# Performance work log

Measured on AMD Instinct MI355X. Metric: run time of the kernel, lower is better.

## Reference

```python
import jax, jax.numpy as jnp
import numpy as np

N_NODES = 100000
N_EDGES = 800000
HIDDEN = 128


def setup_inputs() -> dict:
    key = jax.random.key(0)
    ks = jax.random.split(key, 9)
    h_n = jax.random.normal(ks[0], (N_NODES, HIDDEN), dtype=jnp.float32)
    edge_src = jax.random.randint(ks[1], (N_EDGES,), 0, N_NODES, dtype=jnp.int32)
    edge_dst = jax.random.randint(ks[2], (N_EDGES,), 0, N_NODES, dtype=jnp.int32)
    s = 0.05
    W_w = jax.random.normal(ks[3], (HIDDEN, HIDDEN), dtype=jnp.float32) * s
    W_b = jax.random.normal(ks[4], (HIDDEN,), dtype=jnp.float32) * s
    Ws_w = jax.random.normal(ks[5], (HIDDEN, HIDDEN), dtype=jnp.float32) * s
    Ws_b = jax.random.normal(ks[6], (HIDDEN,), dtype=jnp.float32) * s
    Wt_w = jax.random.normal(ks[7], (HIDDEN, HIDDEN), dtype=jnp.float32) * s
    Wt_b = jax.random.normal(ks[8], (HIDDEN,), dtype=jnp.float32) * s
    return {"h_n": h_n, "edge_src": edge_src, "edge_dst": edge_dst,
            "W_w": W_w, "W_b": W_b, "Ws_w": Ws_w, "Ws_b": Ws_b,
            "Wt_w": Wt_w, "Wt_b": Wt_b}


def reference(h_n, edge_src, edge_dst, W_w, W_b, Ws_w, Ws_b, Wt_w, Wt_b):
    # Dense linears (nn.Linear: x @ W.T + b)
    Wh = h_n @ W_w.T + W_b        # [N,H] used for A @ W(h)
    Wsh = h_n @ Ws_w.T + Ws_b     # [N,H] self term
    Wth = h_n @ Wt_w.T + Wt_b     # [N,H] used for A.T @ W_trans(h)
    # A[src,dst] = 1:  (A @ X)[i]   = sum over edges (i,j) of X[j]
    #              (A.T @ X)[j] = sum over edges (i,j) of X[i]
    agg_fwd = jax.ops.segment_sum(Wh[edge_dst], edge_src, num_segments=N_NODES)
    agg_bwd = jax.ops.segment_sum(Wth[edge_src], edge_dst, num_segments=N_NODES)
    return jax.nn.relu(agg_fwd + Wsh + agg_bwd)
```

## Files before the change

kernel.cpp:

```cpp
#include <hip/hip_runtime.h>
#include <hip/hip_bf16.h>

#define NN 100000
#define NE 800000
#define HIDDEN 128
#define NED (2 * NE)
#define BKN 64
#define NBF 1563
#define NBUCK (2 * NBF)
#define PS 13
#define CHUNK 4096
#define PBLK ((NED + CHUNK - 1) / CHUNK)
#define NTILES 3125

typedef __attribute__((ext_vector_type(8))) short bf16x8;
typedef __attribute__((ext_vector_type(4))) short bf16x4;
typedef __attribute__((ext_vector_type(4))) float f32x4;

__device__ __forceinline__ short f2bf(float f) {
  union { float f; unsigned u; } x; x.f = f;
  unsigned r = x.u + 0x7fffu + ((x.u >> 16) & 1u);
  return (short)(r >> 16);
}
__device__ __forceinline__ float bf2f(short s) {
  union { unsigned u; float f; } x;
  x.u = ((unsigned)(unsigned short)s) << 16;
  return x.f;
}

__global__ __launch_bounds__(256) void convert_weights(
    const float* __restrict__ m0, const float* __restrict__ m1,
    const float* __restrict__ m2, short* __restrict__ out) {
  int i = blockIdx.x * 256 + threadIdx.x;
  int m = i >> 14, j = i & 16383;
  const float* s = (m == 0) ? m0 : (m == 1) ? m1 : m2;
  out[i] = f2bf(s[j]);
}

__global__ __launch_bounds__(256) void convert_h(
    const float* __restrict__ h, short* __restrict__ h_bf) {
  int i = blockIdx.x * 256 + threadIdx.x;
  f32x4 v = *(const f32x4*)(h + (size_t)i * 4);
  bf16x4 o;
#pragma unroll
  for (int j = 0; j < 4; j++) o[j] = f2bf(v[j]);
  *(bf16x4*)(h_bf + (size_t)i * 4) = o;
}

__global__ __launch_bounds__(256) void part_count(
    const int* __restrict__ esrc, const int* __restrict__ edst,
    int* __restrict__ ghist) {
  __shared__ int lh[NBUCK];
  int tid = threadIdx.x;
  for (int i = tid; i < NBUCK; i += 256) lh[i] = 0;
  __syncthreads();
  int base = blockIdx.x * CHUNK;
  int nit = min(CHUNK, NED - base);
  for (int k = tid; k < nit; k += 256) {
    int ed = base + k;
    int b;
    if (ed < NE) b = esrc[ed] >> 6;
    else b = NBF + (edst[ed - NE] >> 6);
    atomicAdd(&lh[b], 1);
  }
  __syncthreads();
  for (int i = tid; i < NBUCK; i += 256) {
    int c = lh[i];
    if (c) atomicAdd(ghist + i, c);
  }
}

__global__ __launch_bounds__(1024) void bucket_scan(
    const int* __restrict__ ghist, int* __restrict__ bstart,
    int* __restrict__ gcur) {
  __shared__ int wsum[16];
  __shared__ int woff[16];
  int tid = threadIdx.x;
  int lane = tid & 63, wv = tid >> 6;
  int base = tid * 4;
  int v0 = (base + 0 < NBUCK) ? ghist[base + 0] : 0;
  int v1 = (base + 1 < NBUCK) ? ghist[base + 1] : 0;
  int v2 = (base + 2 < NBUCK) ? ghist[base + 2] : 0;
  int v3 = (base + 3 < NBUCK) ? ghist[base + 3] : 0;
  int s = v0 + v1 + v2 + v3;
  int inc = s;
#pragma unroll
  for (int d = 1; d < 64; d <<= 1) {
    int t = __shfl_up(inc, d, 64);
    if (lane >= d) inc += t;
  }
  if (lane == 63) wsum[wv] = inc;
  __syncthreads();
  if (wv == 0) {
    int x = (lane < 16) ? wsum[lane] : 0;
    int i2 = x;
#pragma unroll
    for (int d = 1; d < 16; d <<= 1) {
      int t = __shfl_up(i2, d, 64);
      if (lane >= d) i2 += t;
    }
    if (lane < 16) woff[lane] = i2 - x;
  }
  __syncthreads();
  int e = woff[wv] + inc - s;
  if (base + 0 < NBUCK) { bstart[base + 0] = e; gcur[base + 0] = e; }
  e += v0;
  if (base + 1 < NBUCK) { bstart[base + 1] = e; gcur[base + 1] = e; }
  e += v1;
  if (base + 2 < NBUCK) { bstart[base + 2] = e; gcur[base + 2] = e; }
  e += v2;
  if (base + 3 < NBUCK) { bstart[base + 3] = e; gcur[base + 3] = e; }
  e += v3;
  if (tid == 1023) bstart[NBUCK] = e;
}

__global__ __launch_bounds__(256) void part_scatter(
    const int* __restrict__ esrc, const int* __restrict__ edst,
    int* __restrict__ gcur, unsigned* __restrict__ ELP) {
  __shared__ int lcur[NBUCK];
  __shared__ int loff[NBUCK];
  __shared__ int gbase[NBUCK];
  __shared__ int psum[256];
  __shared__ unsigned buf[CHUNK];
  __shared__ unsigned short bidA[CHUNK];
  int tid = threadIdx.x;
  for (int i = tid; i < NBUCK; i += 256) lcur[i] = 0;
  __syncthreads();
  int base = blockIdx.x * CHUNK;
  int nit = min(CHUNK, NED - base);
  for (int k = tid; k < nit; k += 256) {
    int ed = base + k;
    int b;
    if (ed < NE) b = esrc[ed] >> 6;
    else b = NBF + (edst[ed - NE] >> 6);
    atomicAdd(&lcur[b], 1);
  }
  __syncthreads();
  int s = 0;
  int lo0 = tid * PS, hi0 = min(NBUCK, tid * PS + PS);
  for (int j = lo0; j < hi0; j++) s += lcur[j];
  psum[tid] = s;
  __syncthreads();
  for (int off = 1; off < 256; off <<= 1) {
    int x = psum[tid];
    int add = (tid >= off) ? psum[tid - off] : 0;
    __syncthreads();
    psum[tid] = x + add;
    __syncthreads();
  }
  int run = psum[tid] - s;
  for (int j = lo0; j < hi0; j++) { loff[j] = run; run += lcur[j]; }
  __syncthreads();
  for (int b = tid; b < NBUCK; b += 256) {
    int c = lcur[b];
    if (c) gbase[b] = atomicAdd(gcur + b, c);
    lcur[b] = loff[b];
  }
  __syncthreads();
  for (int k = tid; k < nit; k += 256) {
    int ed = base + k;
    int b, tl, nbr;
    if (ed < NE) { int tg = esrc[ed]; nbr = edst[ed]; b = tg >> 6; tl = tg & 63; }
    else { int e = ed - NE; int tg = edst[e]; nbr = esrc[e]; b = NBF + (tg >> 6); tl = tg & 63; }
    int slot = atomicAdd(&lcur[b], 1);
    buf[slot] = ((unsigned)tl << 17) | (unsigned)nbr;
    bidA[slot] = (unsigned short)b;
  }
  __syncthreads();
  for (int i = tid; i < nit; i += 256) {
    int b = bidA[i];
    ELP[gbase[b] + (i - loff[b])] = buf[i];
  }
}

#define ACC8(V) { a0f+=bf2f((V)[0]); a1f+=bf2f((V)[1]); a2f+=bf2f((V)[2]); a3f+=bf2f((V)[3]); \
                  a4f+=bf2f((V)[4]); a5f+=bf2f((V)[5]); a6f+=bf2f((V)[6]); a7f+=bf2f((V)[7]); }
#define MACC8(M,V) { a0f=fmaf(M,bf2f((V)[0]),a0f); a1f=fmaf(M,bf2f((V)[1]),a1f); \
                     a2f=fmaf(M,bf2f((V)[2]),a2f); a3f=fmaf(M,bf2f((V)[3]),a3f); \
                     a4f=fmaf(M,bf2f((V)[4]),a4f); a5f=fmaf(M,bf2f((V)[5]),a5f); \
                     a6f=fmaf(M,bf2f((V)[6]),a6f); a7f=fmaf(M,bf2f((V)[7]),a7f); }
__global__ __launch_bounds__(256, 6) void bucket_gather(
    const short* __restrict__ h_bf, const unsigned* __restrict__ ELP,
    const int* __restrict__ bstart,
    short* __restrict__ aggF, short* __restrict__ aggB,
    int* __restrict__ degFB) {
  __shared__ int sorted[1024];
  __shared__ int cnt[BKN];
  __shared__ int pfx[BKN];
  __shared__ int cur[BKN];
  int tid = threadIdx.x;
  int blk = blockIdx.x;
  int s = bstart[blk], e = bstart[blk + 1], n = e - s;
  if (tid < BKN) cnt[tid] = 0;
  __syncthreads();
  for (int k = tid; k < n; k += 256) atomicAdd(&cnt[ELP[s + k] >> 17], 1);
  __syncthreads();
  int v = (tid < BKN) ? cnt[tid] : 0;
  if (tid < BKN) pfx[tid] = v;
  __syncthreads();
  for (int off = 1; off < BKN; off <<= 1) {
    int add = (tid < BKN && tid >= off) ? pfx[tid - off] : 0;
    __syncthreads();
    if (tid < BKN) pfx[tid] += add;
    __syncthreads();
  }
  if (tid < BKN) cur[tid] = pfx[tid] - cnt[tid];
  __syncthreads();
  for (int k = tid; k < n; k += 256) {
    unsigned pv = ELP[s + k];
    int slot = atomicAdd(&cur[pv >> 17], 1);
    sorted[slot] = (int)(pv & 0x1FFFFu);
  }
  __syncthreads();
  int dir = blk >= NBF;
  int node0 = (dir ? blk - NBF : blk) * BKN;
  short* agg = dir ? aggB : aggF;
  int qw = tid >> 4, q = tid & 15;
  const short* hb = h_bf + (size_t)q * 8;
#pragma unroll
  for (int t = 0; t < 4; t++) {
    int nd = qw * 4 + t;
    int b0 = pfx[nd];
    int deg = cnt[nd];
    int a0 = b0 - deg;
    float a0f = 0.f, a1f = 0.f, a2f = 0.f, a3f = 0.f;
    float a4f = 0.f, a5f = 0.f, a6f = 0.f, a7f = 0.f;
    if (deg > 0) {
      int lastp = b0 - 1;
      int i0 = sorted[a0];
      int i1 = sorted[min(a0 + 1, lastp)];
      int i2 = sorted[min(a0 + 2, lastp)];
      int i3 = sorted[min(a0 + 3, lastp)];
      bf16x8 v0 = *(const bf16x8*)(hb + (size_t)i0 * HIDDEN);
      bf16x8 v1 = *(const bf16x8*)(hb + (size_t)i1 * HIDDEN);
      bf16x8 v2 = *(const bf16x8*)(hb + (size_t)i2 * HIDDEN);
      bf16x8 v3 = *(const bf16x8*)(hb + (size_t)i3 * HIDDEN);
      int j = a0;
      int ni0 = sorted[min(j + 4, lastp)];
      int ni1 = sorted[min(j + 5, lastp)];
      int ni2 = sorted[min(j + 6, lastp)];
      int ni3 = sorted[min(j + 7, lastp)];
      while (j + 4 <= b0) {
        ACC8(v0); v0 = *(const bf16x8*)(hb + (size_t)ni0 * HIDDEN);
        ACC8(v1); v1 = *(const bf16x8*)(hb + (size_t)ni1 * HIDDEN);
        ACC8(v2); v2 = *(const bf16x8*)(hb + (size_t)ni2 * HIDDEN);
        ACC8(v3); v3 = *(const bf16x8*)(hb + (size_t)ni3 * HIDDEN);
        j += 4;
        ni0 = sorted[min(j + 4, lastp)];
        ni1 = sorted[min(j + 5, lastp)];
        ni2 = sorted[min(j + 6, lastp)];
        ni3 = sorted[min(j + 7, lastp)];
      }
      int r = b0 - j;
      float m1 = (r > 0) ? 1.f : 0.f;
      float m2 = (r > 1) ? 1.f : 0.f;
      float m3 = (r > 2) ? 1.f : 0.f;
      MACC8(m1, v0); MACC8(m2, v1); MACC8(m3, v2);
    }
    int node = node0 + nd;
    if (node < NN) {
      bf16x8 o;
      o[0] = f2bf(a0f); o[1] = f2bf(a1f); o[2] = f2bf(a2f); o[3] = f2bf(a3f);
      o[4] = f2bf(a4f); o[5] = f2bf(a5f); o[6] = f2bf(a6f); o[7] = f2bf(a7f);
      *(bf16x8*)(agg + (size_t)node * HIDDEN + q * 8) = o;
    }
  }
  if (tid < BKN) {
    int node = node0 + tid;
    if (node < NN) degFB[dir * NN + node] = cnt[tid];
  }
}

__global__ __launch_bounds__(512, 4) void gemm_fused(
    const short* __restrict__ h_bf, const short* __restrict__ aggF,
    const short* __restrict__ aggB, const short* __restrict__ Wbf,
    const float* __restrict__ Wb, const float* __restrict__ Wsb,
    const float* __restrict__ Wtb, const int* __restrict__ degFB,
    float* __restrict__ out) {
  __shared__ short At[3 * 32 * 136];
  int tid = threadIdx.x;
  int lane = tid & 63;
  int m16 = lane & 15;
  int kq  = lane >> 4;
  int col0 = (tid >> 6) * 16;

  bf16x8 wf[3][4];
#pragma unroll
  for (int i = 0; i < 3; i++)
#pragma unroll
    for (int t = 0; t < 4; t++)
      wf[i][t] = *(const bf16x8*)(Wbf + i * 16384 + (col0 + m16) * 128 + t * 32 + kq * 8);

  f32x4 bW = *(const f32x4*)(Wb  + col0 + kq * 4);
  f32x4 bS = *(const f32x4*)(Wsb + col0 + kq * 4);
  f32x4 bT = *(const f32x4*)(Wtb + col0 + kq * 4);

  int srow = tid >> 4, skc = tid & 15;
  const short* mats[3] = { h_bf, aggF, aggB };
  const short* gbs[3];
  short* lps[3];
#pragma unroll
  for (int k = 0; k < 3; k++) {
    gbs[k] = mats[k] + srow * 128 + skc * 8;
    lps[k] = At + k * 4352 + srow * 136 + skc * 8;
  }

  int tile = blockIdx.x;
  bf16x8 ld[3];
#pragma unroll
  for (int k = 0; k < 3; k++)
    ld[k] = *(const bf16x8*)(gbs[k] + (size_t)tile * 4096);

  while (tile < NTILES) {
    int row0 = tile * 32;
    __syncthreads();
#pragma unroll
    for (int k = 0; k < 3; k++) *(bf16x8*)lps[k] = ld[k];
    __syncthreads();
    int ntile = tile + gridDim.x;
    if (ntile < NTILES) {
#pragma unroll
      for (int k = 0; k < 3; k++)
        ld[k] = *(const bf16x8*)(gbs[k] + (size_t)ntile * 4096);
    }
#pragma unroll
    for (int g = 0; g < 2; g++) {
      f32x4 acc = {0.f, 0.f, 0.f, 0.f};
      const short* lb = At + (g * 16 + m16) * 136 + kq * 8;
#pragma unroll
      for (int i = 0; i < 3; i++)
#pragma unroll
        for (int t = 0; t < 4; t++) {
          bf16x8 af = *(const bf16x8*)(lb + i * 4352 + t * 32);
          acc = __builtin_amdgcn_mfma_f32_16x16x32_bf16(wf[i][t], af, acc, 0, 0, 0);
        }
      int r = row0 + g * 16 + m16;
      float dF = (float)degFB[r];
      float dB = (float)degFB[NN + r];
      f32x4 v;
#pragma unroll
      for (int j = 0; j < 4; j++)
        v[j] = fmaxf(acc[j] + bS[j] + dF * bW[j] + dB * bT[j], 0.f);
      *(f32x4*)(out + (size_t)r * HIDDEN + col0 + kq * 4) = v;
    }
    tile = ntile;
  }
}

extern "C" void kernel_launch(void* const* d_in, const int* in_sizes, int n_in,
                              void* d_out, int out_size, void* d_ws, size_t ws_size,
                              hipStream_t stream) {
  const float* h    = (const float*)d_in[0];
  const int*   esrc = (const int*)d_in[1];
  const int*   edst = (const int*)d_in[2];
  const float* Ww   = (const float*)d_in[3];
  const float* Wb   = (const float*)d_in[4];
  const float* Wsw  = (const float*)d_in[5];
  const float* Wsb  = (const float*)d_in[6];
  const float* Wtw  = (const float*)d_in[7];
  const float* Wtb  = (const float*)d_in[8];
  float* out = (float*)d_out;

  char* ws = (char*)d_ws;
  int*      ghist  = (int*)(ws + 0);
  int*      bstart = (int*)(ws + 12544);
  int*      gcur   = (int*)(ws + 25088);
  unsigned* ELP    = (unsigned*)(ws + 37632);
  short*    Wbf    = (short*)(ws + 6437632);
  short*    h_bf   = (short*)(ws + 6535936);
  short*    aggF   = (short*)(ws + 32135936);
  short*    aggB   = (short*)(ws + 57735936);
  int*      degFB  = (int*)(ws + 83335936);

  hipMemsetAsync(ghist, 0, NBUCK * sizeof(int), stream);

  convert_weights<<<192, 256, 0, stream>>>(Wsw, Ww, Wtw, Wbf);
  convert_h<<<12500, 256, 0, stream>>>(h, h_bf);
  part_count<<<PBLK, 256, 0, stream>>>(esrc, edst, ghist);
  bucket_scan<<<1, 1024, 0, stream>>>(ghist, bstart, gcur);
  part_scatter<<<PBLK, 256, 0, stream>>>(esrc, edst, gcur, ELP);
  bucket_gather<<<NBUCK, 256, 0, stream>>>(h_bf, ELP, bstart, aggF, aggB, degFB);
  gemm_fused<<<1024, 512, 0, stream>>>(
      h_bf, aggF, aggB, Wbf, Wb, Wsb, Wtb, degFB, out);
}
```

Baseline: 258.7 us.

## Fuse bucket gather with GEMM epilogue, merging forward and backward buckets per node block

New measurement: 260.6 us. Within noise of the previous version (+0.8%).

```diff
diff --git a/kernel.cpp b/kernel.cpp
--- a/kernel.cpp
+++ b/kernel.cpp
@@ -7,11 +7,10 @@
 #define NED (2 * NE)
 #define BKN 64
 #define NBF 1563
-#define NBUCK (2 * NBF)
-#define PS 13
+#define NBUCK NBF
+#define PS 7
 #define CHUNK 4096
 #define PBLK ((NED + CHUNK - 1) / CHUNK)
-#define NTILES 3125
 
 typedef __attribute__((ext_vector_type(8))) short bf16x8;
 typedef __attribute__((ext_vector_type(4))) short bf16x4;
@@ -58,9 +57,7 @@
   int nit = min(CHUNK, NED - base);
   for (int k = tid; k < nit; k += 256) {
     int ed = base + k;
-    int b;
-    if (ed < NE) b = esrc[ed] >> 6;
-    else b = NBF + (edst[ed - NE] >> 6);
+    int b = (ed < NE) ? (esrc[ed] >> 6) : (edst[ed - NE] >> 6);
     atomicAdd(&lh[b], 1);
   }
   __syncthreads();
@@ -130,9 +127,7 @@
   int nit = min(CHUNK, NED - base);
   for (int k = tid; k < nit; k += 256) {
     int ed = base + k;
-    int b;
-    if (ed < NE) b = esrc[ed] >> 6;
-    else b = NBF + (edst[ed - NE] >> 6);
+    int b = (ed < NE) ? (esrc[ed] >> 6) : (edst[ed - NE] >> 6);
     atomicAdd(&lcur[b], 1);
   }
   __syncthreads();
@@ -159,11 +154,11 @@
   __syncthreads();
   for (int k = tid; k < nit; k += 256) {
     int ed = base + k;
-    int b, tl, nbr;
-    if (ed < NE) { int tg = esrc[ed]; nbr = edst[ed]; b = tg >> 6; tl = tg & 63; }
-    else { int e = ed - NE; int tg = edst[e]; nbr = esrc[e]; b = NBF + (tg >> 6); tl = tg & 63; }
+    int b, tl, nbr, dir;
+    if (ed < NE) { int tg = esrc[ed]; nbr = edst[ed]; b = tg >> 6; tl = tg & 63; dir = 0; }
+    else { int e = ed - NE; int tg = edst[e]; nbr = esrc[e]; b = tg >> 6; tl = tg & 63; dir = 1; }
     int slot = atomicAdd(&lcur[b], 1);
-    buf[slot] = ((unsigned)tl << 17) | (unsigned)nbr;
+    buf[slot] = ((unsigned)dir << 23) | ((unsigned)tl << 17) | (unsigned)nbr;
     bidA[slot] = (unsigned short)b;
   }
   __syncthreads();
@@ -179,42 +174,48 @@
                      a2f=fmaf(M,bf2f((V)[2]),a2f); a3f=fmaf(M,bf2f((V)[3]),a3f); \
                      a4f=fmaf(M,bf2f((V)[4]),a4f); a5f=fmaf(M,bf2f((V)[5]),a5f); \
                      a6f=fmaf(M,bf2f((V)[6]),a6f); a7f=fmaf(M,bf2f((V)[7]),a7f); }
-__global__ __launch_bounds__(256, 6) void bucket_gather(
+__global__ __launch_bounds__(512, 4) void fused_gather_gemm(
     const short* __restrict__ h_bf, const unsigned* __restrict__ ELP,
-    const int* __restrict__ bstart,
-    short* __restrict__ aggF, short* __restrict__ aggB,
-    int* __restrict__ degFB) {
-  __shared__ int sorted[1024];
-  __shared__ int cnt[BKN];
-  __shared__ int pfx[BKN];
-  __shared__ int cur[BKN];
+    const int* __restrict__ bstart, const short* __restrict__ Wbf,
+    const float* __restrict__ Wb, const float* __restrict__ Wsb,
+    const float* __restrict__ Wtb, float* __restrict__ out) {
+  __shared__ int sorted[2048];
+  __shared__ int cnt[128];
+  __shared__ int pfx[128];
+  __shared__ int cur[128];
+  __shared__ short At[3 * 64 * 136];
   int tid = threadIdx.x;
   int blk = blockIdx.x;
+  int node0 = blk * BKN;
   int s = bstart[blk], e = bstart[blk + 1], n = e - s;
-  if (tid < BKN) cnt[tid] = 0;
-  __syncthreads();
-  for (int k = tid; k < n; k += 256) atomicAdd(&cnt[ELP[s + k] >> 17], 1);
-  __syncthreads();
-  int v = (tid < BKN) ? cnt[tid] : 0;
-  if (tid < BKN) pfx[tid] = v;
-  __syncthreads();
-  for (int off = 1; off < BKN; off <<= 1) {
-    int add = (tid < BKN && tid >= off) ? pfx[tid - off] : 0;
+  if (tid < 128) cnt[tid] = 0;
+  __syncthreads();
+  for (int k = tid; k < n; k += 512) atomicAdd(&cnt[ELP[s + k] >> 17], 1);
+  for (int p = tid; p < 1024; p += 512) {
+    int row = p >> 4, colc = p & 15;
+    int nd = node0 + row;
+    bf16x8 hv = {0, 0, 0, 0, 0, 0, 0, 0};
+    if (nd < NN) hv = *(const bf16x8*)(h_bf + (size_t)nd * HIDDEN + colc * 8);
+    *(bf16x8*)(At + row * 136 + colc * 8) = hv;
+  }
+  __syncthreads();
+  int v = (tid < 128) ? cnt[tid] : 0;
+  if (tid < 128) pfx[tid] = v;
+  __syncthreads();
+  for (int off = 1; off < 128; off <<= 1) {
+    int add = (tid < 128 && tid >= off) ? pfx[tid - off] : 0;
     __syncthreads();
-    if (tid < BKN) pfx[tid] += add;
+    if (tid < 128) pfx[tid] += add;
     __syncthreads();
   }
-  if (tid < BKN) cur[tid] = pfx[tid] - cnt[tid];
-  __syncthreads();
-  for (int k = tid; k < n; k += 256) {
+  if (tid < 128) cur[tid] = pfx[tid] - cnt[tid];
+  __syncthreads();
+  for (int k = tid; k < n; k += 512) {
     unsigned pv = ELP[s + k];
     int slot = atomicAdd(&cur[pv >> 17], 1);
     sorted[slot] = (int)(pv & 0x1FFFFu);
   }
   __syncthreads();
-  int dir = blk >= NBF;
-  int node0 = (dir ? blk - NBF : blk) * BKN;
-  short* agg = dir ? aggB : aggF;
   int qw = tid >> 4, q = tid & 15;
   const short* hb = h_bf + (size_t)q * 8;
 #pragma unroll
@@ -257,93 +258,48 @@
       float m3 = (r > 2) ? 1.f : 0.f;
       MACC8(m1, v0); MACC8(m2, v1); MACC8(m3, v2);
     }
-    int node = node0 + nd;
-    if (node < NN) {
-      bf16x8 o;
-      o[0] = f2bf(a0f); o[1] = f2bf(a1f); o[2] = f2bf(a2f); o[3] = f2bf(a3f);
-      o[4] = f2bf(a4f); o[5] = f2bf(a5f); o[6] = f2bf(a6f); o[7] = f2bf(a7f);
-      *(bf16x8*)(agg + (size_t)node * HIDDEN + q * 8) = o;
-    }
-  }
-  if (tid < BKN) {
-    int node = node0 + tid;
-    if (node < NN) degFB[dir * NN + node] = cnt[tid];
-  }
-}
-
-__global__ __launch_bounds__(512, 4) void gemm_fused(
-    const short* __restrict__ h_bf, const short* __restrict__ aggF,
-    const short* __restrict__ aggB, const short* __restrict__ Wbf,
-    const float* __restrict__ Wb, const float* __restrict__ Wsb,
-    const float* __restrict__ Wtb, const int* __restrict__ degFB,
-    float* __restrict__ out) {
-  __shared__ short At[3 * 32 * 136];
-  int tid = threadIdx.x;
+    short* dst = At + (1 + (nd >> 6)) * 8704 + (nd & 63) * 136 + q * 8;
+    bf16x8 o;
+    o[0] = f2bf(a0f); o[1] = f2bf(a1f); o[2] = f2bf(a2f); o[3] = f2bf(a3f);
+    o[4] = f2bf(a4f); o[5] = f2bf(a5f); o[6] = f2bf(a6f); o[7] = f2bf(a7f);
+    *(bf16x8*)dst = o;
+  }
+  __syncthreads();
   int lane = tid & 63;
   int m16 = lane & 15;
   int kq  = lane >> 4;
   int col0 = (tid >> 6) * 16;
-
   bf16x8 wf[3][4];
 #pragma unroll
   for (int i = 0; i < 3; i++)
 #pragma unroll
     for (int t = 0; t < 4; t++)
       wf[i][t] = *(const bf16x8*)(Wbf + i * 16384 + (col0 + m16) * 128 + t * 32 + kq * 8);
-
   f32x4 bW = *(const f32x4*)(Wb  + col0 + kq * 4);
   f32x4 bS = *(const f32x4*)(Wsb + col0 + kq * 4);
   f32x4 bT = *(const f32x4*)(Wtb + col0 + kq * 4);
-
-  int srow = tid >> 4, skc = tid & 15;
-  const short* mats[3] = { h_bf, aggF, aggB };
-  const short* gbs[3];
-  short* lps[3];
-#pragma unroll
-  for (int k = 0; k < 3; k++) {
-    gbs[k] = mats[k] + srow * 128 + skc * 8;
-    lps[k] = At + k * 4352 + srow * 136 + skc * 8;
-  }
-
-  int tile = blockIdx.x;
-  bf16x8 ld[3];
-#pragma unroll
-  for (int k = 0; k < 3; k++)
-    ld[k] = *(const bf16x8*)(gbs[k] + (size_t)tile * 4096);
-
-  while (tile < NTILES) {
-    int row0 = tile * 32;
-    __syncthreads();
-#pragma unroll
-    for (int k = 0; k < 3; k++) *(bf16x8*)lps[k] = ld[k];
-    __syncthreads();
-    int ntile = tile + gridDim.x;
-    if (ntile < NTILES) {
-#pragma unroll
-      for (int k = 0; k < 3; k++)
-        ld[k] = *(const bf16x8*)(gbs[k] + (size_t)ntile * 4096);
+#pragma unroll
+  for (int g = 0; g < 4; g++) {
+    f32x4 acc = {0.f, 0.f, 0.f, 0.f};
+    const short* lb = At + (g * 16 + m16) * 136 + kq * 8;
+#pragma unroll
+    for (int i = 0; i < 3; i++)
+#pragma unroll
+      for (int t = 0; t < 4; t++) {
+        bf16x8 af = *(const bf16x8*)(lb + i * 8704 + t * 32);
+        acc = __builtin_amdgcn_mfma_f32_16x16x32_bf16(wf[i][t], af, acc, 0, 0, 0);
+      }
+    int rl = g * 16 + m16;
+    int r = node0 + rl;
+    if (r < NN) {
+      float dF = (float)cnt[rl];
+      float dB = (float)cnt[64 + rl];
+      f32x4 vv;
+#pragma unroll
+      for (int j = 0; j < 4; j++)
+        vv[j] = fmaxf(acc[j] + bS[j] + dF * bW[j] + dB * bT[j], 0.f);
+      *(f32x4*)(out + (size_t)r * HIDDEN + col0 + kq * 4) = vv;
     }
-#pragma unroll
-    for (int g = 0; g < 2; g++) {
-      f32x4 acc = {0.f, 0.f, 0.f, 0.f};
-      const short* lb = At + (g * 16 + m16) * 136 + kq * 8;
-#pragma unroll
-      for (int i = 0; i < 3; i++)
-#pragma unroll
-        for (int t = 0; t < 4; t++) {
-          bf16x8 af = *(const bf16x8*)(lb + i * 4352 + t * 32);
-          acc = __builtin_amdgcn_mfma_f32_16x16x32_bf16(wf[i][t], af, acc, 0, 0, 0);
-        }
-      int r = row0 + g * 16 + m16;
-      float dF = (float)degFB[r];
-      float dB = (float)degFB[NN + r];
-      f32x4 v;
-#pragma unroll
-      for (int j = 0; j < 4; j++)
-        v[j] = fmaxf(acc[j] + bS[j] + dF * bW[j] + dB * bT[j], 0.f);
-      *(f32x4*)(out + (size_t)r * HIDDEN + col0 + kq * 4) = v;
-    }
-    tile = ntile;
   }
 }
 
@@ -363,14 +319,11 @@
 
   char* ws = (char*)d_ws;
   int*      ghist  = (int*)(ws + 0);
-  int*      bstart = (int*)(ws + 12544);
-  int*      gcur   = (int*)(ws + 25088);
-  unsigned* ELP    = (unsigned*)(ws + 37632);
-  short*    Wbf    = (short*)(ws + 6437632);
-  short*    h_bf   = (short*)(ws + 6535936);
-  short*    aggF   = (short*)(ws + 32135936);
-  short*    aggB   = (short*)(ws + 57735936);
-  int*      degFB  = (int*)(ws + 83335936);
+  int*      bstart = (int*)(ws + 6272);
+  int*      gcur   = (int*)(ws + 12544);
+  unsigned* ELP    = (unsigned*)(ws + 18816);
+  short*    Wbf    = (short*)(ws + 6418816);
+  short*    h_bf   = (short*)(ws + 6517120);
 
   hipMemsetAsync(ghist, 0, NBUCK * sizeof(int), stream);
 
@@ -379,7 +332,6 @@
   part_count<<<PBLK, 256, 0, stream>>>(esrc, edst, ghist);
   bucket_scan<<<1, 1024, 0, stream>>>(ghist, bstart, gcur);
   part_scatter<<<PBLK, 256, 0, stream>>>(esrc, edst, gcur, ELP);
-  bucket_gather<<<NBUCK, 256, 0, stream>>>(h_bf, ELP, bstart, aggF, aggB, degFB);
-  gemm_fused<<<1024, 512, 0, stream>>>(
-      h_bf, aggF, aggB, Wbf, Wb, Wsb, Wtb, degFB, out);
-}
+  fused_gather_gemm<<<NBF, 512, 0, stream>>>(
+      h_bf, ELP, bstart, Wbf, Wb, Wsb, Wtb, out);
+}
```
